# Performance work log

Hardware: AMD Instinct MI355X
Metric: run time of the kernel (lower is better)

Reference implementation:

```python
import jax, jax.numpy as jnp
import numpy as np

# Episode / graph constants
B, N, K, Q = 16, 5, 5, 5              # episodes, ways, shots, queries-per-class
NPG = 200                              # nodes per graph
DEG = 16                               # avg degree
F_DIM, H_DIM, OUT_DIM = 128, 128, 64
NS_G = B * N * K                       # 400 support graphs
NQ_G = B * N * Q                       # 400 query graphs
NS_NODES = NS_G * NPG                  # 80000
NQ_NODES = NQ_G * NPG                  # 80000
NEG_SLOPE = 0.2


def _rand_edges(key, n_nodes):
    # random in-graph source per (dst, k) slot; dst covers every node DEG times
    n_edges = n_nodes * DEG
    off = (jnp.arange(n_edges) // (NPG * DEG)) * NPG
    src = jax.random.randint(key, (n_edges,), 0, NPG) + off
    dst = jnp.repeat(jnp.arange(n_nodes), DEG)
    return jnp.stack([src, dst]).astype(jnp.int64)


def setup_inputs() -> dict:
    key = jax.random.key(0)
    ks = jax.random.split(key, 16)
    g = lambda k, shape, scale: jax.random.normal(k, shape, jnp.float32) * scale
    inp = {
        "supports_x": g(ks[0], (NS_NODES, F_DIM), 1.0),
        "queries_x": g(ks[1], (NQ_NODES, F_DIM), 1.0),
        "supports_edge_index": _rand_edges(ks[2], NS_NODES),
        "queries_edge_index": _rand_edges(ks[3], NQ_NODES),
        "supports_batch": (jnp.arange(NS_NODES) // NPG).astype(jnp.int64),
        "queries_batch": (jnp.arange(NQ_NODES) // NPG).astype(jnp.int64),
        # per-episode labels: N classes, K graphs each, local class ids 0..N-1
        "supports_y": jnp.tile(jnp.repeat(jnp.arange(N), K), B).astype(jnp.int64),
        "W1": g(ks[4], (F_DIM, H_DIM), 1.0 / np.sqrt(F_DIM)),
        "a1_src": g(ks[5], (H_DIM,), 1.0 / np.sqrt(H_DIM)),
        "a1_dst": g(ks[6], (H_DIM,), 1.0 / np.sqrt(H_DIM)),
        "b1": jnp.zeros((H_DIM,), jnp.float32),
        "W2": g(ks[7], (H_DIM, H_DIM), 1.0 / np.sqrt(H_DIM)),
        "a2_src": g(ks[8], (H_DIM,), 1.0 / np.sqrt(H_DIM)),
        "a2_dst": g(ks[9], (H_DIM,), 1.0 / np.sqrt(H_DIM)),
        "b2": jnp.zeros((H_DIM,), jnp.float32),
        "Wm1": g(ks[10], (H_DIM, H_DIM), 1.0 / np.sqrt(H_DIM)),
        "bm1": jnp.zeros((H_DIM,), jnp.float32),
        "Wm2": g(ks[11], (H_DIM, OUT_DIM), 1.0 / np.sqrt(H_DIM)),
        "bm2": jnp.zeros((OUT_DIM,), jnp.float32),
    }
    return inp


def gat_conv(x, src, dst, W, a_src, a_dst, b, n_nodes):
    """PyG GATConv, heads=1, add_self_loops=True."""
    xw = x @ W                                        # [n, H]
    loop = jnp.arange(n_nodes)
    src2 = jnp.concatenate([src, loop])
    dst2 = jnp.concatenate([dst, loop])
    e = (xw @ a_src)[src2] + (xw @ a_dst)[dst2]       # [E+n]
    e = jnp.where(e > 0, e, NEG_SLOPE * e)            # leaky_relu
    m = jax.ops.segment_max(e, dst2, num_segments=n_nodes)
    ex = jnp.exp(e - m[dst2])
    den = jax.ops.segment_sum(ex, dst2, num_segments=n_nodes)
    alpha = ex / den[dst2]                            # softmax per destination
    out = jax.ops.segment_sum(alpha[:, None] * xw[src2], dst2, num_segments=n_nodes)
    return out + b


def embed(x, edge_index, batch, n_graphs, W1, a1s, a1d, b1, W2, a2s, a2d, b2,
          Wm1, bm1, Wm2, bm2):
    n = x.shape[0]
    src, dst = edge_index[0], edge_index[1]
    h = jax.nn.relu(gat_conv(x, src, dst, W1, a1s, a1d, b1, n))
    h = jax.nn.relu(gat_conv(h, src, dst, W2, a2s, a2d, b2, n))
    h = jax.nn.relu(h @ Wm1 + bm1) @ Wm2 + bm2        # MLP
    # global mean pool
    s = jax.ops.segment_sum(h, batch, num_segments=n_graphs)
    cnt = jax.ops.segment_sum(jnp.ones((n,), h.dtype), batch, num_segments=n_graphs)
    return s / cnt[:, None]                           # [n_graphs, OUT_DIM]


def reference(supports_x, supports_edge_index, supports_batch, supports_y,
              queries_x, queries_edge_index, queries_batch,
              W1, a1_src, a1_dst, b1, W2, a2_src, a2_dst, b2,
              Wm1, bm1, Wm2, bm2):
    params = (W1, a1_src, a1_dst, b1, W2, a2_src, a2_dst, b2, Wm1, bm1, Wm2, bm2)
    emb_s = embed(supports_x, supports_edge_index, supports_batch, NS_G, *params)
    emb_q = embed(queries_x, queries_edge_index, queries_batch, NQ_G, *params)

    # class prototypes per episode: mean of supports with each (sorted) class label
    emb_s = emb_s.reshape(B, N * K, OUT_DIM)
    y = supports_y.reshape(B, N * K)
    onehot = jax.nn.one_hot(y, N, dtype=emb_s.dtype)          # [B, NK, N]
    proto = jnp.einsum("bkn,bke->bne", onehot, emb_s)
    proto = proto / onehot.sum(axis=1)[:, :, None]            # [B, N, E]

    # align queries with prototypes
    nq = N * Q                                                # queries per episode
    emb_q = emb_q.reshape(B, nq, OUT_DIM)
    rep_q = jnp.repeat(emb_q, N, axis=1)                      # repeat_interleave
    rep_p = jnp.tile(proto, (1, nq, 1))                       # repeat
    return rep_q.reshape(B * nq * N, OUT_DIM), rep_p.reshape(B * nq * N, OUT_DIM)
```

## Files before the change

### kernel.cpp

```cpp
#include <hip/hip_runtime.h>


typedef unsigned short u16;
typedef unsigned int   u32;
typedef unsigned char  u8;
typedef __attribute__((ext_vector_type(8))) short short8;
typedef __attribute__((ext_vector_type(4))) float f32x4;

#define NNODES   80000
#define DEG      16
#define NEDGES   (NNODES * DEG)
#define NGRAPH   400
#define NPG      200
#define FDIM     128
#define ODIM     64
#define NEPS     16
#define NWAY     5
#define NSHOT    5
#define NROWS    (2 * NNODES)
#define NGR2     (2 * NGRAPH)

__device__ __forceinline__ float b2f(u16 u) {
    return __uint_as_float(((u32)u) << 16);
}
__device__ __forceinline__ u16 f2b(float f) {
    u32 i = __float_as_uint(f);
    u32 r = i + 0x7FFFu + ((i >> 16) & 1u);
    return (u16)(r >> 16);
}
__device__ __forceinline__ u32 cvtpk(float lo, float hi) {
    u32 r;
    asm("v_cvt_pk_bf16_f32 %0, %1, %2" : "=v"(r) : "v"(lo), "v"(hi));
    return r;
}
__device__ __forceinline__ int semk(int p) {
    return 16 * ((p >> 2) & 7) + 4 * (p >> 5) + 2 * ((p >> 1) & 1) + (p & 1);
}

__global__ void detect_kernel(const u32* __restrict__ sx,
                              const int* __restrict__ ei,
                              int* __restrict__ flags)
{
    if (blockIdx.x == 0 && threadIdx.x == 0) {
        int ok32 = (ei[NEDGES + 16000] == 1000) && (ei[NEDGES + 32000] == 2000);
        flags[0] = ok32 ? 0 : 1;
        int cnt = 0;
        for (int i = 0; i < 64; i++) {
            u32 lo = sx[i] & 0xFFFFu;
            u32 e  = (lo >> 7) & 0xFFu;
            if (e >= 110u && e <= 135u) cnt++;
        }
        flags[1] = (cnt >= 32) ? 1 : 0;
    }
}

__global__ __launch_bounds__(256)
void canon_kernel(const void* __restrict__ W1, const void* __restrict__ W2,
                  const void* __restrict__ Wm1, const void* __restrict__ Wm2,
                  const void* a1s, const void* a1d, const void* b1,
                  const void* a2s, const void* a2d, const void* b2,
                  const void* bm1, const void* bm2,
                  const int* __restrict__ flags, u16* __restrict__ Wc,
                  float* __restrict__ Vc, float* __restrict__ emb)
{
    const int b = blockIdx.x, t = threadIdx.x;
    const int isb = flags[1];
    if (b < 224) {
        int idx = b * 256 + t;
        const void* src;
        int n, k, nout;
        if (idx < 16384)      { src = W1;  int l = idx;         n = l >> 7; k = l & 127;       nout = 128; }
        else if (idx < 32768) { src = W2;  int l = idx - 16384; n = l >> 7; k = semk(l & 127); nout = 128; }
        else if (idx < 49152) { src = Wm1; int l = idx - 32768; n = l >> 7; k = semk(l & 127); nout = 128; }
        else                  { src = Wm2; int l = idx - 49152; n = l >> 7; k = semk(l & 127); nout = 64; }
        int off = k * nout + n;
        Wc[idx] = isb ? ((const u16*)src)[off] : f2b(((const float*)src)[off]);
    } else if (b == 224) {
        for (int idx = t; idx < 960; idx += 256) {
            int g = idx >> 7, off = idx & 127;
            const void* src = (g == 0) ? a1s : (g == 1) ? a1d : (g == 2) ? b1 :
                              (g == 3) ? a2s : (g == 4) ? a2d : (g == 5) ? b2 :
                              (g == 6) ? bm1 : bm2;
            int soff = (g == 2 || g == 5) ? semk(off) : off;
            Vc[idx] = isb ? b2f(((const u16*)src)[soff]) : ((const float*)src)[soff];
        }
    } else {
        int i = (b - 225) * 256 + t;
        emb[i] = 0.f;
    }
}

__global__ __launch_bounds__(512)
void gemm_pack_kernel(const void* __restrict__ in0, const void* __restrict__ in1,
                      int in_mode, const int* __restrict__ flags,
                      const u16* __restrict__ Wt, const float* __restrict__ bias,
                      const float* __restrict__ avs, const float* __restrict__ avd,
                      u32* __restrict__ outP, float* __restrict__ es_g,
                      float* __restrict__ ed_g, int do_relu)
{
    __shared__ __align__(16) uint4 bsh[2304];

    const int t    = threadIdx.x;
    const int wv   = t >> 6;
    const int lane = t & 63;
    const int qd   = lane >> 4, md = lane & 15;
    const int lofs = lane + (lane >> 3);

    int mode = in_mode;
    if (mode == 2) mode = flags[1];

    const size_t rowG = (size_t)blockIdx.x * 128 + wv * 16 + md;
    const int side = rowG >= NNODES;
    const size_t lrow = rowG - (side ? NNODES : 0);
    const void* in_ = side ? in1 : in0;

    short8 afr[4];
    if (mode) {
        const short* arow = (const short*)in_ + lrow * FDIM;
#pragma unroll
        for (int ks = 0; ks < 4; ks++)
            afr[ks] = *(const short8*)(arow + ks * 32 + qd * 8);
    } else {
        const float* arow = (const float*)in_ + lrow * FDIM;
#pragma unroll
        for (int ks = 0; ks < 4; ks++) {
            float4 u = *(const float4*)(arow + ks * 32 + qd * 8);
            float4 v = *(const float4*)(arow + ks * 32 + qd * 8 + 4);
            short8 tt;
            tt[0] = (short)f2b(u.x); tt[1] = (short)f2b(u.y);
            tt[2] = (short)f2b(u.z); tt[3] = (short)f2b(u.w);
            tt[4] = (short)f2b(v.x); tt[5] = (short)f2b(v.y);
            tt[6] = (short)f2b(v.z); tt[7] = (short)f2b(v.w);
            afr[ks] = tt;
        }
    }

    {
        const uint4* w4 = (const uint4*)Wt;
#pragma unroll
        for (int it = 0; it < 4; ++it) {
            int u    = it * 512 + t;
            int ctb  = u >> 8, mdb = (u >> 4) & 15, ksb = (u >> 2) & 3, qdb = u & 3;
            int slot = ctb * 256 + ksb * 64 + qdb * 16 + mdb;
            bsh[slot + (slot >> 3)] = w4[u];
        }
    }
    __syncthreads();

    const bool has_av = (avs != nullptr);
    float sv = 0.f, dv = 0.f;
    u32 ov[16];

#pragma unroll
    for (int ct = 0; ct < 8; ct++) {
        f32x4 acc = {0.f, 0.f, 0.f, 0.f};
#pragma unroll
        for (int ks = 0; ks < 4; ks++) {
            short8 bfr = *(const short8*)&bsh[(ct * 4 + ks) * 72 + lofs];
            acc = __builtin_amdgcn_mfma_f32_16x16x32_bf16(bfr, afr[ks], acc, 0, 0, 0);
        }
        const int colb = ct * 16 + qd * 4;
        float4 bv4 = make_float4(0.f, 0.f, 0.f, 0.f);
        if (bias) bv4 = *(const float4*)&bias[colb];
        float v0 = acc[0] + bv4.x;
        float v1 = acc[1] + bv4.y;
        float v2 = acc[2] + bv4.z;
        float v3 = acc[3] + bv4.w;
        if (do_relu) {
            v0 = fmaxf(v0, 0.f); v1 = fmaxf(v1, 0.f);
            v2 = fmaxf(v2, 0.f); v3 = fmaxf(v3, 0.f);
        }
        if (has_av) {
            float4 as4 = *(const float4*)&avs[colb];
            float4 ad4 = *(const float4*)&avd[colb];
            sv = fmaf(v0, as4.x, sv); sv = fmaf(v1, as4.y, sv);
            sv = fmaf(v2, as4.z, sv); sv = fmaf(v3, as4.w, sv);
            dv = fmaf(v0, ad4.x, dv); dv = fmaf(v1, ad4.y, dv);
            dv = fmaf(v2, ad4.z, dv); dv = fmaf(v3, ad4.w, dv);
        }
        ov[ct * 2]     = cvtpk(v0, v1);
        ov[ct * 2 + 1] = cvtpk(v2, v3);
    }

    {
        u32* orow = outP + rowG * 64 + qd * 16;
#pragma unroll
        for (int k4 = 0; k4 < 4; ++k4) {
            uint4 o;
            o.x = ov[k4 * 4]; o.y = ov[k4 * 4 + 1];
            o.z = ov[k4 * 4 + 2]; o.w = ov[k4 * 4 + 3];
            *(uint4*)&orow[k4 * 4] = o;
        }
    }

    if (has_av) {
        sv += __shfl_xor(sv, 16, 64);  dv += __shfl_xor(dv, 16, 64);
        sv += __shfl_xor(sv, 32, 64);  dv += __shfl_xor(dv, 32, 64);
        if (qd == 0) {
            es_g[rowG] = sv;
            ed_g[rowG] = dv;
        }
    }
}

__global__ __launch_bounds__(512)
void gemm_pool_kernel(const u32* __restrict__ inP, const u16* __restrict__ Wt,
                      float* __restrict__ emb)
{
    __shared__ uint4 bsh[1024];
    __shared__ float psum[2][8][64];

    const int t = threadIdx.x;
    const int wv   = t >> 6;
    const int lane = t & 63;
    const int qd   = lane >> 4, md = lane & 15;

    const size_t rowA = (size_t)blockIdx.x * 128 + wv * 16 + md;
    const short* arow = (const short*)inP + rowA * FDIM;
    short8 afr[4];
#pragma unroll
    for (int ks = 0; ks < 4; ks++)
        afr[ks] = *(const short8*)(arow + ks * 32 + qd * 8);

    {
        const uint4* w4 = (const uint4*)Wt;
#pragma unroll
        for (int it = 0; it < 2; ++it) {
            int u   = it * 512 + t;
            int ctb = u >> 8, mdb = (u >> 4) & 15, ksb = (u >> 2) & 3, qdb = u & 3;
            bsh[ctb * 256 + ksb * 64 + qdb * 16 + mdb] = w4[u];
        }
    }
    __syncthreads();

    const int r0       = blockIdx.x * 128 + wv * 16 + qd * 4;
    const int g0       = (blockIdx.x * 128) / NPG;
    const int boundary = (g0 + 1) * NPG;

    for (int ct = 0; ct < 4; ct++) {
        f32x4 acc = {0.f, 0.f, 0.f, 0.f};
#pragma unroll
        for (int ks = 0; ks < 4; ks++) {
            short8 bfr = *(const short8*)&bsh[(ct * 4 + ks) * 64 + lane];
            acc = __builtin_amdgcn_mfma_f32_16x16x32_bf16(afr[ks], bfr, acc, 0, 0, 0);
        }
        float s0 = 0.f, s1 = 0.f;
#pragma unroll
        for (int i = 0; i < 4; i++) {
            if (r0 + i >= boundary) s1 += acc[i];
            else                    s0 += acc[i];
        }
        s0 += __shfl_xor(s0, 16, 64);  s1 += __shfl_xor(s1, 16, 64);
        s0 += __shfl_xor(s0, 32, 64);  s1 += __shfl_xor(s1, 32, 64);
        if (qd == 0) {
            psum[0][wv][ct * 16 + md] = s0;
            psum[1][wv][ct * 16 + md] = s1;
        }
    }
    __syncthreads();

    if (t < 128) {
        int p = t >> 6, c = t & 63;
        float s = 0.f;
#pragma unroll
        for (int w = 0; w < 8; w++) s += psum[p][w][c];
        if (p == 0 || boundary < blockIdx.x * 128 + 128)
            atomicAdd(&emb[(size_t)(g0 + p) * ODIM + c], s * (1.f / (float)NPG));
    }
}

__global__ __launch_bounds__(1024)
void gat_kernel(const u32* __restrict__ xwP, const float* __restrict__ es_g,
                const float* __restrict__ ed_g, const int* __restrict__ src0,
                const int* __restrict__ src1, const int* __restrict__ flags,
                const float* __restrict__ bias, u32* __restrict__ outH)
{
    __shared__ __align__(16) u32 xls[NPG * 64];
    __shared__ u16 alA[NPG * 18];
    __shared__ u8  slA[NPG * 20];

    const int g = blockIdx.x, t = threadIdx.x;
    const int side  = g >= NGRAPH;
    const int gbase = g * NPG;
    const int lbase = (g - (side ? NGRAPH : 0)) * NPG;
    const int* __restrict__ src = side ? src1 : src0;

    {
        const u32* gsrc = xwP + (size_t)gbase * 64;
        const int w = t >> 6, l = t & 63;
#pragma unroll
        for (int it = 0; it < 4; ++it) {
            int chunk = w + it * 16;
            if (chunk < 50) {
                __builtin_amdgcn_global_load_lds(
                    (const u32*)(gsrc + chunk * 256 + l * 4),
                    &xls[chunk * 256], 16, 0, 0);
            }
        }
    }

    if (t < 4 * NPG) {
        const int n = t >> 2, slot = t & 3;
        const int j0 = slot * 5;
        const int jn = (slot == 3) ? 2 : 5;
        const int is64 = flags[0];
        const float edn = ed_g[gbase + n];
        int   sl[5];
        float e[5];
        float mx = -1e30f;
#pragma unroll
        for (int jj = 0; jj < 5; jj++) {
            if (jj < jn) {
                int j = j0 + jj;
                int s;
                if (j == 16) {
                    s = n;
                } else {
                    int eidx = (lbase + n) * DEG + j;
                    s = (is64 ? src[2 * eidx] : src[eidx]) - lbase;
                }
                sl[jj] = s;
                float ev = es_g[gbase + s] + edn;
                ev = (ev > 0.f) ? ev : 0.2f * ev;
                e[jj] = ev;
                mx = fmaxf(mx, ev);
            }
        }
        mx = fmaxf(mx, __shfl_xor(mx, 1, 64));
        mx = fmaxf(mx, __shfl_xor(mx, 2, 64));
        float den = 0.f;
#pragma unroll
        for (int jj = 0; jj < 5; jj++) {
            if (jj < jn) {
                e[jj] = __expf(e[jj] - mx);
                den += e[jj];
            }
        }
        den += __shfl_xor(den, 1, 64);
        den += __shfl_xor(den, 2, 64);
        const float inv = 65535.f / den;
#pragma unroll
        for (int jj = 0; jj < 5; jj++) {
            if (jj < jn) {
                alA[n * 18 + j0 + jj] = (u16)(e[jj] * inv + 0.5f);
                slA[n * 20 + j0 + jj] = (u8)sl[jj];
            }
        }
    }

    __syncthreads();

    const int w = t >> 6, l = t & 63;
    const int sub = l >> 4, li = l & 15;
    const float4 bz0 = *(const float4*)&bias[8 * li];
    const float4 bz1 = *(const float4*)&bias[8 * li + 4];

    for (int p = w; p < NPG / 4; p += 16) {
        const int n = 4 * p + sub;
        float h0 = 0.f, h1 = 0.f, h2 = 0.f, h3 = 0.f;
        float h4 = 0.f, h5 = 0.f, h6 = 0.f, h7 = 0.f;
#pragma unroll 4
        for (int j = 0; j < 17; j++) {
            float a = (float)alA[n * 18 + j] * (1.f / 65535.f);
            int   s = (int)slA[n * 20 + j];
            uint4 q = *(const uint4*)&xls[s * 64 + 4 * li];
            h0 = fmaf(a, __uint_as_float(q.x << 16), h0);
            h1 = fmaf(a, __uint_as_float(q.x & 0xFFFF0000u), h1);
            h2 = fmaf(a, __uint_as_float(q.y << 16), h2);
            h3 = fmaf(a, __uint_as_float(q.y & 0xFFFF0000u), h3);
            h4 = fmaf(a, __uint_as_float(q.z << 16), h4);
            h5 = fmaf(a, __uint_as_float(q.z & 0xFFFF0000u), h5);
            h6 = fmaf(a, __uint_as_float(q.w << 16), h6);
            h7 = fmaf(a, __uint_as_float(q.w & 0xFFFF0000u), h7);
        }
        h0 = fmaxf(h0 + bz0.x, 0.f);
        h1 = fmaxf(h1 + bz0.y, 0.f);
        h2 = fmaxf(h2 + bz0.z, 0.f);
        h3 = fmaxf(h3 + bz0.w, 0.f);
        h4 = fmaxf(h4 + bz1.x, 0.f);
        h5 = fmaxf(h5 + bz1.y, 0.f);
        h6 = fmaxf(h6 + bz1.z, 0.f);
        h7 = fmaxf(h7 + bz1.w, 0.f);
        uint4 o;
        o.x = cvtpk(h0, h1);
        o.y = cvtpk(h2, h3);
        o.z = cvtpk(h4, h5);
        o.w = cvtpk(h6, h7);
        *(uint4*)&outH[(size_t)(gbase + n) * 64 + 4 * li] = o;
    }
}

__global__ __launch_bounds__(256)
void expand_kernel(const float* __restrict__ emb, const float* __restrict__ bm2,
                   const int* __restrict__ flags, void* __restrict__ out)
{
    int idx = blockIdx.x * 256 + threadIdx.x;
    const int TOT = NEPS * 125 * ODIM;
    if (idx >= TOT) return;
    int c = idx & 63;
    int tq = (idx >> 6) % 125;
    int b = idx / (125 * ODIM);
    int q = tq / NWAY, n = tq % NWAY;
    const float bb = bm2[c];
    float v0 = emb[(size_t)(NGRAPH + b * 25 + q) * ODIM + c] + bb;
    float v1 = 0.f;
#pragma unroll
    for (int k = 0; k < NSHOT; k++)
        v1 += emb[(size_t)(b * 25 + n * NSHOT + k) * ODIM + c];
    v1 = v1 * (1.f / (float)NSHOT) + bb;
    if (flags[1]) {
        ((u16*)out)[idx]       = f2b(v0);
        ((u16*)out)[TOT + idx] = f2b(v1);
    } else {
        ((float*)out)[idx]       = v0;
        ((float*)out)[TOT + idx] = v1;
    }
}

extern "C" void kernel_launch(void* const* d_in, const int* in_sizes, int n_in,
                              void* d_out, int out_size, void* d_ws, size_t ws_size,
                              hipStream_t stream)
{
    const void* sup_x  = d_in[0];
    const void* qry_x  = d_in[1];
    const int*  sup_ei = (const int*)d_in[2];
    const int*  qry_ei = (const int*)d_in[3];
    const void* W1  = d_in[7];
    const void* a1s = d_in[8];
    const void* a1d = d_in[9];
    const void* b1  = d_in[10];
    const void* W2  = d_in[11];
    const void* a2s = d_in[12];
    const void* a2d = d_in[13];
    const void* b2  = d_in[14];
    const void* Wm1 = d_in[15];
    const void* bm1 = d_in[16];
    const void* Wm2 = d_in[17];
    const void* bm2 = d_in[18];

    u32*   bufXW = (u32*)d_ws;
    u32*   bufH  = bufXW + (size_t)NROWS * 64;
    float* es_g  = (float*)(bufH + (size_t)NROWS * 64);
    float* ed_g  = es_g + NROWS;
    float* emb   = ed_g + NROWS;
    float* Vc    = emb + (size_t)NGR2 * ODIM;
    u16*   Wc    = (u16*)(Vc + 960);
    int*   flags = (int*)(Wc + 57344);

    const float* c_a1s = Vc + 0,   *c_a1d = Vc + 128, *c_b1  = Vc + 256;
    const float* c_a2s = Vc + 384, *c_a2d = Vc + 512, *c_b2  = Vc + 640;
    const float* c_bm1 = Vc + 768, *c_bm2 = Vc + 896;
    const u16* c_W1t  = Wc;
    const u16* c_W2t  = Wc + 16384;
    const u16* c_Wm1t = Wc + 32768;
    const u16* c_Wm2t = Wc + 49152;

    const int GEMM_BLOCKS = NROWS / 128;

    detect_kernel<<<1, 64, 0, stream>>>((const u32*)sup_x, sup_ei, flags);
    canon_kernel<<<425, 256, 0, stream>>>(W1, W2, Wm1, Wm2,
                                          a1s, a1d, b1, a2s, a2d, b2, bm1, bm2,
                                          flags, Wc, Vc, emb);

    const void* bufH0 = (const void*)bufH;
    const void* bufH1 = (const void*)(bufH + (size_t)NNODES * 64);

    gemm_pack_kernel<<<GEMM_BLOCKS, 512, 0, stream>>>(
        sup_x, qry_x, 2, flags, c_W1t, nullptr, c_a1s, c_a1d,
        bufXW, es_g, ed_g, 0);
    gat_kernel<<<NGR2, 1024, 0, stream>>>(
        bufXW, es_g, ed_g, sup_ei, qry_ei, flags, c_b1, bufH);

    gemm_pack_kernel<<<GEMM_BLOCKS, 512, 0, stream>>>(
        bufH0, bufH1, 1, flags, c_W2t, nullptr, c_a2s, c_a2d,
        bufXW, es_g, ed_g, 0);
    gat_kernel<<<NGR2, 1024, 0, stream>>>(
        bufXW, es_g, ed_g, sup_ei, qry_ei, flags, c_b2, bufH);

    gemm_pack_kernel<<<GEMM_BLOCKS, 512, 0, stream>>>(
        bufH0, bufH1, 1, flags, c_Wm1t, c_bm1, nullptr, nullptr,
        bufXW, es_g, ed_g, 1);

    gemm_pool_kernel<<<GEMM_BLOCKS, 512, 0, stream>>>(bufXW, c_Wm2t, emb);

    expand_kernel<<<(NEPS * 125 * ODIM + 255) / 256, 256, 0, stream>>>(
        emb, c_bm2, flags, d_out);
}
```

Baseline: 312.3 us.

## Store intermediate features as four column planes and split GAT per graph into halves

Intermediate bf16 feature buffers now use a plane-split layout: four planes of 32 columns each, instead of row-major 128-column rows. The GEMM kernels read and write these planes, and a new mode 3 reads from the plane buffer. The GAT aggregation kernel now launches two 512-thread blocks per graph, and each block handles one 64-column half. Each block loads only its half into LDS, which cuts shared memory per block and should raise occupancy and parallelism. The cost is that attention softmax coefficients are computed twice per graph, once in each half-block, and each thread now handles 9 edge slots instead of 5.

```diff
diff --git a/kernel.cpp b/kernel.cpp
--- a/kernel.cpp
+++ b/kernel.cpp
@@ -19,6 +19,7 @@
 #define NSHOT    5
 #define NROWS    (2 * NNODES)
 #define NGR2     (2 * NGRAPH)
+#define PLANE    (NROWS * 16)
 
 __device__ __forceinline__ float b2f(u16 u) {
     return __uint_as_float(((u32)u) << 16);
@@ -110,28 +111,35 @@
     if (mode == 2) mode = flags[1];
 
     const size_t rowG = (size_t)blockIdx.x * 128 + wv * 16 + md;
-    const int side = rowG >= NNODES;
-    const size_t lrow = rowG - (side ? NNODES : 0);
-    const void* in_ = side ? in1 : in0;
 
     short8 afr[4];
-    if (mode) {
-        const short* arow = (const short*)in_ + lrow * FDIM;
+    if (mode == 3) {
+        const u32* ap = (const u32*)in0 + rowG * 16;
 #pragma unroll
         for (int ks = 0; ks < 4; ks++)
-            afr[ks] = *(const short8*)(arow + ks * 32 + qd * 8);
+            afr[ks] = *(const short8*)(ap + (size_t)ks * PLANE + qd * 4);
     } else {
-        const float* arow = (const float*)in_ + lrow * FDIM;
-#pragma unroll
-        for (int ks = 0; ks < 4; ks++) {
-            float4 u = *(const float4*)(arow + ks * 32 + qd * 8);
-            float4 v = *(const float4*)(arow + ks * 32 + qd * 8 + 4);
-            short8 tt;
-            tt[0] = (short)f2b(u.x); tt[1] = (short)f2b(u.y);
-            tt[2] = (short)f2b(u.z); tt[3] = (short)f2b(u.w);
-            tt[4] = (short)f2b(v.x); tt[5] = (short)f2b(v.y);
-            tt[6] = (short)f2b(v.z); tt[7] = (short)f2b(v.w);
-            afr[ks] = tt;
+        const int side = rowG >= NNODES;
+        const size_t lrow = rowG - (side ? NNODES : 0);
+        const void* in_ = side ? in1 : in0;
+        if (mode == 1) {
+            const short* arow = (const short*)in_ + lrow * FDIM;
+#pragma unroll
+            for (int ks = 0; ks < 4; ks++)
+                afr[ks] = *(const short8*)(arow + ks * 32 + qd * 8);
+        } else {
+            const float* arow = (const float*)in_ + lrow * FDIM;
+#pragma unroll
+            for (int ks = 0; ks < 4; ks++) {
+                float4 u = *(const float4*)(arow + ks * 32 + qd * 8);
+                float4 v = *(const float4*)(arow + ks * 32 + qd * 8 + 4);
+                short8 tt;
+                tt[0] = (short)f2b(u.x); tt[1] = (short)f2b(u.y);
+                tt[2] = (short)f2b(u.z); tt[3] = (short)f2b(u.w);
+                tt[4] = (short)f2b(v.x); tt[5] = (short)f2b(v.y);
+                tt[6] = (short)f2b(v.z); tt[7] = (short)f2b(v.w);
+                afr[ks] = tt;
+            }
         }
     }
 
@@ -183,13 +191,13 @@
     }
 
     {
-        u32* orow = outP + rowG * 64 + qd * 16;
+        u32* op = outP + (size_t)qd * PLANE + rowG * 16;
 #pragma unroll
         for (int k4 = 0; k4 < 4; ++k4) {
             uint4 o;
             o.x = ov[k4 * 4]; o.y = ov[k4 * 4 + 1];
             o.z = ov[k4 * 4 + 2]; o.w = ov[k4 * 4 + 3];
-            *(uint4*)&orow[k4 * 4] = o;
+            *(uint4*)&op[k4 * 4] = o;
         }
     }
 
@@ -216,11 +224,11 @@
     const int qd   = lane >> 4, md = lane & 15;
 
     const size_t rowA = (size_t)blockIdx.x * 128 + wv * 16 + md;
-    const short* arow = (const short*)inP + rowA * FDIM;
+    const u32* ap = inP + rowA * 16;
     short8 afr[4];
 #pragma unroll
     for (int ks = 0; ks < 4; ks++)
-        afr[ks] = *(const short8*)(arow + ks * 32 + qd * 8);
+        afr[ks] = *(const short8*)(ap + (size_t)ks * PLANE + qd * 4);
 
     {
         const uint4* w4 = (const uint4*)Wt;
@@ -269,47 +277,51 @@
     }
 }
 
-__global__ __launch_bounds__(1024)
+__global__ __launch_bounds__(512)
 void gat_kernel(const u32* __restrict__ xwP, const float* __restrict__ es_g,
                 const float* __restrict__ ed_g, const int* __restrict__ src0,
                 const int* __restrict__ src1, const int* __restrict__ flags,
                 const float* __restrict__ bias, u32* __restrict__ outH)
 {
-    __shared__ __align__(16) u32 xls[NPG * 64];
+    __shared__ __align__(16) u32 xls[2][208][16];
     __shared__ u16 alA[NPG * 18];
     __shared__ u8  slA[NPG * 20];
 
-    const int g = blockIdx.x, t = threadIdx.x;
+    const int bid = blockIdx.x, t = threadIdx.x;
+    const int g = bid >> 1, h = bid & 1;
     const int side  = g >= NGRAPH;
     const int gbase = g * NPG;
     const int lbase = (g - (side ? NGRAPH : 0)) * NPG;
     const int* __restrict__ src = side ? src1 : src0;
 
     {
-        const u32* gsrc = xwP + (size_t)gbase * 64;
         const int w = t >> 6, l = t & 63;
 #pragma unroll
         for (int it = 0; it < 4; ++it) {
-            int chunk = w + it * 16;
-            if (chunk < 50) {
+            int chunk = w + it * 8;
+            if (chunk < 26) {
+                int qi = (chunk < 13) ? 0 : 1;
+                int c  = chunk - qi * 13;
+                const u32* gsrc = xwP + (size_t)(2 * h + qi) * PLANE
+                                + (size_t)(gbase) * 16 + c * 256;
                 __builtin_amdgcn_global_load_lds(
-                    (const u32*)(gsrc + chunk * 256 + l * 4),
-                    &xls[chunk * 256], 16, 0, 0);
+                    (const u32*)(gsrc + l * 4),
+                    &xls[qi][c * 16][0], 16, 0, 0);
             }
         }
     }
 
-    if (t < 4 * NPG) {
-        const int n = t >> 2, slot = t & 3;
-        const int j0 = slot * 5;
-        const int jn = (slot == 3) ? 2 : 5;
+    if (t < 2 * NPG) {
+        const int n = t >> 1, slot = t & 1;
+        const int j0 = slot ? 9 : 0;
+        const int jn = slot ? 8 : 9;
         const int is64 = flags[0];
         const float edn = ed_g[gbase + n];
-        int   sl[5];
-        float e[5];
+        int   sl[9];
+        float e[9];
         float mx = -1e30f;
 #pragma unroll
-        for (int jj = 0; jj < 5; jj++) {
+        for (int jj = 0; jj < 9; jj++) {
             if (jj < jn) {
                 int j = j0 + jj;
                 int s;
@@ -327,20 +339,18 @@
             }
         }
         mx = fmaxf(mx, __shfl_xor(mx, 1, 64));
-        mx = fmaxf(mx, __shfl_xor(mx, 2, 64));
         float den = 0.f;
 #pragma unroll
-        for (int jj = 0; jj < 5; jj++) {
+        for (int jj = 0; jj < 9; jj++) {
             if (jj < jn) {
                 e[jj] = __expf(e[jj] - mx);
                 den += e[jj];
             }
         }
         den += __shfl_xor(den, 1, 64);
-        den += __shfl_xor(den, 2, 64);
         const float inv = 65535.f / den;
 #pragma unroll
-        for (int jj = 0; jj < 5; jj++) {
+        for (int jj = 0; jj < 9; jj++) {
             if (jj < jn) {
                 alA[n * 18 + j0 + jj] = (u16)(e[jj] * inv + 0.5f);
                 slA[n * 20 + j0 + jj] = (u8)sl[jj];
@@ -352,41 +362,31 @@
 
     const int w = t >> 6, l = t & 63;
     const int sub = l >> 4, li = l & 15;
-    const float4 bz0 = *(const float4*)&bias[8 * li];
-    const float4 bz1 = *(const float4*)&bias[8 * li + 4];
-
-    for (int p = w; p < NPG / 4; p += 16) {
+    const int hq = li >> 3, li7 = li & 7;
+    const float4 bz = *(const float4*)&bias[h * 64 + li * 4];
+
+    for (int p = w; p < NPG / 4; p += 8) {
         const int n = 4 * p + sub;
         float h0 = 0.f, h1 = 0.f, h2 = 0.f, h3 = 0.f;
-        float h4 = 0.f, h5 = 0.f, h6 = 0.f, h7 = 0.f;
 #pragma unroll 4
         for (int j = 0; j < 17; j++) {
             float a = (float)alA[n * 18 + j] * (1.f / 65535.f);
             int   s = (int)slA[n * 20 + j];
-            uint4 q = *(const uint4*)&xls[s * 64 + 4 * li];
+            uint2 q = *(const uint2*)&xls[hq][s][li7 * 2];
             h0 = fmaf(a, __uint_as_float(q.x << 16), h0);
             h1 = fmaf(a, __uint_as_float(q.x & 0xFFFF0000u), h1);
             h2 = fmaf(a, __uint_as_float(q.y << 16), h2);
             h3 = fmaf(a, __uint_as_float(q.y & 0xFFFF0000u), h3);
-            h4 = fmaf(a, __uint_as_float(q.z << 16), h4);
-            h5 = fmaf(a, __uint_as_float(q.z & 0xFFFF0000u), h5);
-            h6 = fmaf(a, __uint_as_float(q.w << 16), h6);
-            h7 = fmaf(a, __uint_as_float(q.w & 0xFFFF0000u), h7);
-        }
-        h0 = fmaxf(h0 + bz0.x, 0.f);
-        h1 = fmaxf(h1 + bz0.y, 0.f);
-        h2 = fmaxf(h2 + bz0.z, 0.f);
-        h3 = fmaxf(h3 + bz0.w, 0.f);
-        h4 = fmaxf(h4 + bz1.x, 0.f);
-        h5 = fmaxf(h5 + bz1.y, 0.f);
-        h6 = fmaxf(h6 + bz1.z, 0.f);
-        h7 = fmaxf(h7 + bz1.w, 0.f);
-        uint4 o;
+        }
+        h0 = fmaxf(h0 + bz.x, 0.f);
+        h1 = fmaxf(h1 + bz.y, 0.f);
+        h2 = fmaxf(h2 + bz.z, 0.f);
+        h3 = fmaxf(h3 + bz.w, 0.f);
+        uint2 o;
         o.x = cvtpk(h0, h1);
         o.y = cvtpk(h2, h3);
-        o.z = cvtpk(h4, h5);
-        o.w = cvtpk(h6, h7);
-        *(uint4*)&outH[(size_t)(gbase + n) * 64 + 4 * li] = o;
+        *(uint2*)&outH[(size_t)(2 * h + hq) * PLANE
+                       + (size_t)(gbase + n) * 16 + li7 * 2] = o;
     }
 }
 
@@ -439,8 +439,8 @@
     const void* bm2 = d_in[18];
 
     u32*   bufXW = (u32*)d_ws;
-    u32*   bufH  = bufXW + (size_t)NROWS * 64;
-    float* es_g  = (float*)(bufH + (size_t)NROWS * 64);
+    u32*   bufH  = bufXW + (size_t)4 * PLANE;
+    float* es_g  = (float*)(bufH + (size_t)4 * PLANE);
     float* ed_g  = es_g + NROWS;
     float* emb   = ed_g + NROWS;
     float* Vc    = emb + (size_t)NGR2 * ODIM;
@@ -462,23 +462,20 @@
                                           a1s, a1d, b1, a2s, a2d, b2, bm1, bm2,
                                           flags, Wc, Vc, emb);
 
-    const void* bufH0 = (const void*)bufH;
-    const void* bufH1 = (const void*)(bufH + (size_t)NNODES * 64);
-
     gemm_pack_kernel<<<GEMM_BLOCKS, 512, 0, stream>>>(
         sup_x, qry_x, 2, flags, c_W1t, nullptr, c_a1s, c_a1d,
         bufXW, es_g, ed_g, 0);
-    gat_kernel<<<NGR2, 1024, 0, stream>>>(
+    gat_kernel<<<2 * NGR2, 512, 0, stream>>>(
         bufXW, es_g, ed_g, sup_ei, qry_ei, flags, c_b1, bufH);
 
     gemm_pack_kernel<<<GEMM_BLOCKS, 512, 0, stream>>>(
-        bufH0, bufH1, 1, flags, c_W2t, nullptr, c_a2s, c_a2d,
+        bufH, nullptr, 3, flags, c_W2t, nullptr, c_a2s, c_a2d,
         bufXW, es_g, ed_g, 0);
-    gat_kernel<<<NGR2, 1024, 0, stream>>>(
+    gat_kernel<<<2 * NGR2, 512, 0, stream>>>(
         bufXW, es_g, ed_g, sup_ei, qry_ei, flags, c_b2, bufH);
 
     gemm_pack_kernel<<<GEMM_BLOCKS, 512, 0, stream>>>(
-        bufH0, bufH1, 1, flags, c_Wm1t, c_bm1, nullptr, nullptr,
+        bufH, nullptr, 3, flags, c_Wm1t, c_bm1, nullptr, nullptr,
         bufXW, es_g, ed_g, 1);
 
     gemm_pool_kernel<<<GEMM_BLOCKS, 512, 0, stream>>>(bufXW, c_Wm2t, emb);
```

New measurement: 323.7 us. +3.7%, slower.
